# Performance work log

Hardware: AMD Instinct MI355X
Metric: run time of the kernel (lower is better)

## Reference

```python
import jax, jax.numpy as jnp
import numpy as np

N_SIGMA = 1
K_INST = 8  # instance ids 1..K_INST (0 = background)
W_INST, W_VAR, W_SEED = 1.0, 10.0, 1.0
FG_WEIGHT = 1.0


def make_xym(h, w):
    # torch buffer: linspace(0,2,2048) x / linspace(0,1,1024) y, sliced to [0:h,0:w]
    xm = jnp.linspace(0.0, 2.0, 2048)[:w]
    ym = jnp.linspace(0.0, 1.0, 1024)[:h]
    return jnp.stack([jnp.broadcast_to(xm[None, :], (h, w)),
                      jnp.broadcast_to(ym[:, None], (h, w))], axis=0)  # [2,h,w]


def lovasz_hinge_flat(logits, labels):
    # logits, labels: [N] float (labels in {0,1})
    signs = 2.0 * labels - 1.0
    errors = 1.0 - logits * signs
    order = jnp.argsort(-errors)            # descending sort of errors
    errors_sorted = errors[order]
    gt_sorted = labels[order]
    gts = gt_sorted.sum()
    inter = gts - jnp.cumsum(gt_sorted)
    union = gts + jnp.cumsum(1.0 - gt_sorted)
    jac = 1.0 - inter / union
    grad = jnp.concatenate([jac[:1], jac[1:] - jac[:-1]])
    # torch impl wraps grad in Variable() -> no gradient through grad
    return jnp.dot(jax.nn.relu(errors_sorted), jax.lax.stop_gradient(grad))


def spatial_emb_loss(predictions, instances):
    B, C, T, h, w = predictions.shape
    xym = make_xym(h, w)
    # Faithful to the torch source: due to loop indentation, only the last
    # time step's var/instance/seed losses survive, and obj_count == 1.
    pred = predictions[:, :, T - 1]          # [B,C,h,w]
    inst = instances[:, 0, T - 1]            # [B,h,w] int
    spatial_emb = jnp.tanh(pred[:, 0:2]) + xym[None]   # [B,2,h,w]
    sigma = pred[:, 2:2 + N_SIGMA]                     # [B,1,h,w]
    seed = jax.nn.sigmoid(pred[:, 2 + N_SIGMA])        # [B,h,w]
    npix = float(h * w)

    def per_image(se, sig, sd, ins):
        bg_loss = jnp.sum(jnp.where(ins == 0, sd ** 2, 0.0))

        def per_id(k):
            m = (ins == k).astype(se.dtype)            # [h,w]
            cnt = m.sum()
            safe = jnp.maximum(cnt, 1.0)
            # to_center=True: center of in-mask pixel coordinates
            center = jnp.sum(xym * m[None], axis=(1, 2)) / safe      # [2]
            s_mean = jnp.sum(sig * m[None], axis=(1, 2)) / safe      # [n_sigma]
            var_l = jnp.sum(m[None] * (sig - jax.lax.stop_gradient(s_mean)[:, None, None]) ** 2) / (safe * N_SIGMA)
            s_exp = jnp.exp(s_mean * 10.0)
            dist = jnp.exp(-jnp.sum((se - center[:, None, None]) ** 2 * s_exp[:, None, None], axis=0))  # [h,w]
            inst_l = lovasz_hinge_flat((dist * 2.0 - 1.0).reshape(-1), m.reshape(-1))
            seed_l = FG_WEIGHT * jnp.sum(m * (sd - jax.lax.stop_gradient(dist)) ** 2)
            present = (cnt > 0).astype(se.dtype)       # torch skips absent ids
            return present * var_l, present * inst_l, present * seed_l

        var_l, inst_l, seed_l = jax.vmap(per_id)(jnp.arange(1, K_INST + 1))
        seed_loss = (bg_loss + seed_l.sum()) / npix
        # obj_count == 1 in the original code (incremented once per t-loop)
        return W_INST * inst_l.sum() + W_VAR * var_l.sum() + W_SEED * seed_loss

    per_b = jax.vmap(per_image)(spatial_emb, sigma, seed, inst)
    # torch: loss = loss / b, with b == B-1 after the loop
    return per_b.sum() / (B - 1)


def setup_inputs():
    key = jax.random.key(0)
    k1, k2 = jax.random.split(key)
    B, C, T, H, W = 4, 4, 2, 512, 1024
    predictions = jax.random.normal(k1, (B, C, T, H, W), dtype=jnp.float32)
    instances = jax.random.randint(k2, (B, 1, T, H, W), 0, K_INST + 1, dtype=jnp.int32)
    labels = jnp.zeros((B, 1, T, H, W), dtype=jnp.int32)  # unused by forward
    return {"predictions": predictions, "instances": instances, "labels": labels}


def reference(predictions, instances, labels):
    return spatial_emb_loss(predictions, instances)
```

## Files before the change

kernel.cpp:

```cpp
#include <hip/hip_runtime.h>

#define H 512
#define WID 1024
#define HW (H*WID)
#define B 4
#define K 8
#define NB 1024
#define NBLK1 128

#define OFF_LOSS  0
#define OFF_FIN   16
#define OFF_SPART 512
#define OFF_RED   (OFF_SPART + B*K*NBLK1*5)
#define OFF_PART  (OFF_RED + 2*B*K*NB)

static __device__ __forceinline__ float frcp(float x){
#if __has_builtin(__builtin_amdgcn_rcpf)
  return __builtin_amdgcn_rcpf(x);
#else
  return 1.0f / x;
#endif
}
static __device__ __forceinline__ float fexp2(float x){
#if __has_builtin(__builtin_amdgcn_exp2f)
  return __builtin_amdgcn_exp2f(x);
#else
  return exp2f(x);
#endif
}
static __device__ __forceinline__ float ftanh(float x){
  return 1.0f - 2.0f * frcp(__expf(2.0f*x) + 1.0f);
}
static __device__ __forceinline__ float fsigmoid(float x){
  return frcp(1.0f + __expf(-x));
}

__global__ __launch_bounds__(512) void k1_stats(const float* __restrict__ pred,
                                                const int* __restrict__ inst,
                                                float* __restrict__ ws) {
  const int b = blockIdx.y;
  __shared__ int4   ti[1024];
  __shared__ float4 ts[1024];
  __shared__ float  part5[K][5];
  const float4* sig4 = (const float4*)(pred + (size_t)(8*b + 5) * HW);
  const int4*   ins4 = (const int4*)(inst + (size_t)(2*b + 1) * HW);
  const int base4 = blockIdx.x * 1024;
  #pragma unroll
  for (int i = 0; i < 2; i++) {
    const int q = threadIdx.x + i*512;
    ti[q] = ins4[base4 + q];
    ts[q] = sig4[base4 + q];
  }
  __syncthreads();
  const int wv = threadIdx.x >> 6, lane = threadIdx.x & 63;
  const int kk = wv + 1;
  float cnt=0.f, sx=0.f, sy=0.f, ss=0.f, ss2=0.f;
  #pragma unroll
  for (int j = 0; j < 16; j++) {
    const int q = lane + 64*j;
    const int4   iv = ti[q];
    const float4 sv = ts[q];
    const int p = (base4 + q) * 4;
    const float xm0 = (float)(p & (WID-1)) * (2.0f/2047.0f);
    const float ym  = (float)(p >> 10)     * (1.0f/1023.0f);
    const float m0 = (iv.x==kk)?1.f:0.f, m1=(iv.y==kk)?1.f:0.f,
                m2 = (iv.z==kk)?1.f:0.f, m3=(iv.w==kk)?1.f:0.f;
    const float msum = (m0+m1)+(m2+m3);
    cnt += msum;
    sx  += msum*xm0 + (m1 + 2.0f*m2 + 3.0f*m3)*(2.0f/2047.0f);
    sy  += msum*ym;
    ss  += m0*sv.x + m1*sv.y + m2*sv.z + m3*sv.w;
    ss2 += m0*sv.x*sv.x + m1*sv.y*sv.y + m2*sv.z*sv.z + m3*sv.w*sv.w;
  }
  #pragma unroll
  for (int o=1;o<64;o<<=1){
    cnt+=__shfl_xor(cnt,o,64);
    sx +=__shfl_xor(sx, o,64);
    sy +=__shfl_xor(sy, o,64);
    ss +=__shfl_xor(ss, o,64);
    ss2+=__shfl_xor(ss2,o,64);
  }
  if (lane == 0) {
    part5[wv][0]=cnt; part5[wv][1]=sx; part5[wv][2]=sy; part5[wv][3]=ss; part5[wv][4]=ss2;
  }
  __syncthreads();
  if (threadIdx.x < K*5) {
    const int w = threadIdx.x / 5, c = threadIdx.x % 5;
    ws[OFF_SPART + ((size_t)(b*K + w)*NBLK1 + blockIdx.x)*5 + c] = part5[w][c];
  }
}

__global__ __launch_bounds__(256) void k2_fin(float* __restrict__ ws) {
  const int t = threadIdx.x;
  const int bk = t >> 3, s = t & 7;
  float a0=0.f,a1=0.f,a2=0.f,a3=0.f,a4=0.f;
  for (int j = 0; j < NBLK1/8; j++) {
    const float* p = ws + OFF_SPART + ((size_t)bk*NBLK1 + (s + 8*j))*5;
    a0+=p[0]; a1+=p[1]; a2+=p[2]; a3+=p[3]; a4+=p[4];
  }
  #pragma unroll
  for (int o=1;o<8;o<<=1){
    a0+=__shfl_xor(a0,o,64); a1+=__shfl_xor(a1,o,64); a2+=__shfl_xor(a2,o,64);
    a3+=__shfl_xor(a3,o,64); a4+=__shfl_xor(a4,o,64);
  }
  __shared__ float vloc[32];
  if (s == 0) {
    const float cnt=a0, sx=a1, sy=a2, ss=a3, ss2=a4;
    const float present = (cnt > 0.0f) ? 1.0f : 0.0f;
    const float safe = fmaxf(cnt, 1.0f);
    const float cx = sx/safe, cy = sy/safe, sm = ss/safe;
    const float var = (ss2 - 2.0f*sm*ss + sm*sm*cnt)/safe;
    const float sexp = expf(10.0f * sm);
    const float L2E = 1.4426950408889634f;
    float* fin = ws + OFF_FIN + bk*8;
    fin[0] = -sexp*L2E;
    fin[1] =  2.0f*sexp*cx*L2E;
    fin[2] =  2.0f*sexp*cy*L2E;
    fin[3] = -sexp*(cx*cx + cy*cy)*L2E + 10.0f;
    fin[4] = cnt;
    vloc[bk] = present * 10.0f * var * (1.0f/3.0f);
  }
  __syncthreads();
  if (t == 0) {
    float v = 0.f;
    #pragma unroll
    for (int i = 0; i < 32; i++) v += vloc[i];
    atomicAdd(ws + OFF_LOSS, v);
  }
}

template<int G>
__global__ __launch_bounds__(256, 4) void k3_main(const float* __restrict__ pred,
                                                  const int* __restrict__ inst,
                                                  float* __restrict__ ws,
                                                  unsigned int* __restrict__ part) {
  const int b = blockIdx.y, g = blockIdx.x;
  __shared__ unsigned int hist[K*NB];
  for (int i = threadIdx.x; i < K*NB; i += 256) hist[i] = 0;
  float4 fr[K];
  #pragma unroll
  for (int k=0;k<K;k++){
    const float* fin = ws + OFF_FIN + (b*K + k)*8;
    fr[k] = make_float4(fin[0], fin[1], fin[2], fin[3]);
  }
  __syncthreads();
  const float4* p0 = (const float4*)(pred + (size_t)(8*b+1)*HW);
  const float4* p1 = (const float4*)(pred + (size_t)(8*b+3)*HW);
  const float4* p3 = (const float4*)(pred + (size_t)(8*b+7)*HW);
  const int4*   in4 = (const int4*)(inst + (size_t)(2*b+1)*HW);
  float sAcc = 0.0f;
  constexpr int CH4 = HW / (G*4);
  const int base4 = g * CH4;
  #pragma unroll
  for (int q0 = 0; q0 < CH4; q0 += 256) {
    const int idx = base4 + q0 + threadIdx.x;
    const int4   iv = in4[idx];
    const float4 f0 = p0[idx];
    const float4 f1 = p1[idx];
    const float4 f3 = p3[idx];
    const int p = idx * 4;
    const float xm0 = (float)(p & (WID-1)) * (2.0f/2047.0f);
    const float ym  = (float)(p >> 10)     * (1.0f/1023.0f);
    const int ivv[4] = {iv.x, iv.y, iv.z, iv.w};
    float pxv[4], pyv[4], t2v[4], down[4];
    {
      const float a0v[4] = {f0.x, f0.y, f0.z, f0.w};
      const float a1v[4] = {f1.x, f1.y, f1.z, f1.w};
      #pragma unroll
      for (int e=0;e<4;e++){
        pxv[e] = ftanh(a0v[e]) + xm0 + (float)e*(2.0f/2047.0f);
        pyv[e] = ftanh(a1v[e]) + ym;
        t2v[e] = pxv[e]*pxv[e] + pyv[e]*pyv[e];
        down[e] = 0.0f;
      }
    }
    #pragma unroll
    for (int j=0;j<K;j++){
      const float4 f = fr[j];
      int buv[4]; unsigned addv[4];
      #pragma unroll
      for (int e=0;e<4;e++){
        const float u = fmaf(f.x, t2v[e], fmaf(f.y, pxv[e], fmaf(f.z, pyv[e], f.w)));
        const float v = fexp2(u);
        int vi = (int)v; vi = (vi > NB-1) ? NB-1 : vi;
        const bool own = (ivv[e] == j+1);
        if (own) down[e] = v;
        buv[e] = own ? (NB-1 - vi) : vi;
        addv[e] = own ? 0x10001u : 1u;
      }
      int cur = buv[0]; unsigned acc = addv[0];
      #pragma unroll
      for (int e=1;e<4;e++){
        const bool same = (buv[e] == cur);
        if (!same) atomicAdd(&hist[j*NB + cur], acc);
        acc = same ? acc + addv[e] : addv[e];
        cur = buv[e];
      }
      atomicAdd(&hist[j*NB + cur], acc);
    }
    {
      const float sdv[4] = {fsigmoid(f3.x), fsigmoid(f3.y), fsigmoid(f3.z), fsigmoid(f3.w)};
      #pragma unroll
      for (int e=0;e<4;e++){
        const float d  = (ivv[e] == 0) ? 0.0f : down[e] * (1.0f/1024.0f);
        const float df = sdv[e] - d;
        sAcc += df*df;
      }
    }
  }
  __syncthreads();
  unsigned int* dst = part + ((size_t)b*G + g)*(K*NB);
  for (int i = threadIdx.x; i < K*NB; i += 256) dst[i] = hist[i];
  #pragma unroll
  for (int o=1;o<64;o<<=1) sAcc += __shfl_xor(sAcc, o, 64);
  __shared__ float wsum[4];
  if ((threadIdx.x & 63) == 0) wsum[threadIdx.x>>6] = sAcc;
  __syncthreads();
  if (threadIdx.x == 0) {
    const float tot = wsum[0]+wsum[1]+wsum[2]+wsum[3];
    atomicAdd(ws + OFF_LOSS, tot * (1.0f/((float)HW * 3.0f)));
  }
}

__global__ __launch_bounds__(128) void k4a_reduce(const unsigned int* __restrict__ part,
                                                  unsigned int* __restrict__ red, int G) {
  const int bk = blockIdx.x, c = blockIdx.y;
  const int b = bk >> 3, k = bk & 7;
  const int bu = c*128 + threadIdx.x;
  const unsigned int* base = part + (size_t)b*G*K*NB + (size_t)k*NB + bu;
  unsigned int rc = 0, rp = 0;
  #pragma unroll 8
  for (int g = 0; g < G; g++) {
    const unsigned int v = base[(size_t)g*K*NB];
    rc += v & 0xFFFFu;
    rp += v >> 16;
  }
  red[bk*NB + bu]            = rc;
  red[B*K*NB + bk*NB + bu]   = rp;
}

__global__ __launch_bounds__(256) void k4b_lovasz(const unsigned int* __restrict__ red,
                                                   float* __restrict__ ws) {
  const int bk = blockIdx.x;
  const float cntF = ws[OFF_FIN + bk*8 + 4];
  if (cntF <= 0.0f) return;
  const double Pd = (double)cntF;
  const int t = threadIdx.x;
  const int lane = t & 63, wv = t >> 6;
  unsigned int cnt[4], pos[4];
  #pragma unroll
  for (int j = 0; j < 4; j++) {
    const int bu = NB-1 - (t*4 + j);
    cnt[j] = red[bk*NB + bu];
    pos[j] = red[B*K*NB + bk*NB + bu];
  }
  const int lc = (int)(cnt[0]+cnt[1]+cnt[2]+cnt[3]);
  const int lp = (int)(pos[0]+pos[1]+pos[2]+pos[3]);
  int ic = lc, ip = lp;
  #pragma unroll
  for (int o=1;o<64;o<<=1){
    const int vc = __shfl_up(ic, o, 64);
    const int vp = __shfl_up(ip, o, 64);
    if (lane >= o) { ic += vc; ip += vp; }
  }
  __shared__ int wtc[4], wtp[4];
  if (lane == 63) { wtc[wv] = ic; wtp[wv] = ip; }
  __syncthreads();
  int offc = 0, offp = 0;
  for (int w = 0; w < wv; w++) { offc += wtc[w]; offp += wtp[w]; }
  int irun = offc + ic - lc;
  int crun = offp + ip - lp;
  double acc = 0.0;
  #pragma unroll
  for (int j = 0; j < 4; j++) {
    const int n = (int)cnt[j];
    if (n) {
      const int bu = NB-1 - (t*4 + j);
      const double jac0 = (irun==0) ? 0.0 : 1.0 - (Pd - crun)/(Pd + irun - crun);
      irun += n; crun += (int)pos[j];
      const double jac1 = 1.0 - (Pd - crun)/(Pd + irun - crun);
      acc += ((bu + 0.5) * (2.0/NB)) * (jac1 - jac0);
    }
  }
  #pragma unroll
  for (int o=1;o<64;o<<=1) acc += __shfl_xor(acc, o, 64);
  __shared__ double racc[4];
  if (lane == 0) racc[wv] = acc;
  __syncthreads();
  if (t == 0) {
    const double tot = racc[0]+racc[1]+racc[2]+racc[3];
    atomicAdd(ws + OFF_LOSS, (float)(tot * (1.0/3.0)));
  }
}

__global__ void k5_out(const float* __restrict__ ws, float* __restrict__ out) {
  if (threadIdx.x == 0) out[0] = ws[OFF_LOSS];
}

extern "C" void kernel_launch(void* const* d_in, const int* in_sizes, int n_in,
                              void* d_out, int out_size, void* d_ws, size_t ws_size,
                              hipStream_t stream) {
  const float* pred = (const float*)d_in[0];
  const int*   inst = (const int*)d_in[1];
  float* ws  = (float*)d_ws;
  float* out = (float*)d_out;
  unsigned int* red  = ((unsigned int*)d_ws) + OFF_RED;
  unsigned int* part = ((unsigned int*)d_ws) + OFF_PART;
  int G = 256;
  while (G > 32 && ws_size < ((size_t)OFF_PART + (size_t)B*G*K*NB)*4) G >>= 1;
  hipMemsetAsync(d_ws, 0, (size_t)OFF_FIN*4 + 64, stream);
  k1_stats<<<dim3(NBLK1,B), 512, 0, stream>>>(pred, inst, ws);
  k2_fin  <<<1, 256, 0, stream>>>(ws);
  if      (G == 256) k3_main<256><<<dim3(256,B), 256, 0, stream>>>(pred, inst, ws, part);
  else if (G == 128) k3_main<128><<<dim3(128,B), 256, 0, stream>>>(pred, inst, ws, part);
  else if (G ==  64) k3_main< 64><<<dim3( 64,B), 256, 0, stream>>>(pred, inst, ws, part);
  else               k3_main< 32><<<dim3( 32,B), 256, 0, stream>>>(pred, inst, ws, part);
  k4a_reduce<<<dim3(B*K, 8), 128, 0, stream>>>(part, red, G);
  k4b_lovasz<<<B*K, 256, 0, stream>>>(red, ws);
  k5_out  <<<1, 64, 0, stream>>>(ws, out);
}
```

Before: 149.1 us.

## Fold stats finalize into main kernel, fuse output write, use 512-thread blocks

Removes the separate k2_fin launch: each k3_main block now reduces the k1 partial stats itself (one wave per instance id) and derives its coefficients in shared memory. The final output copy moves into k4b_lovasz through a last-block ticket counter, which drops the k5 launch. The main kernel goes from 256 to 512 threads with half as many blocks, and histogram init and copy use vector stores. The cost is that every k3 block repeats the finalize work, and the larger blocks change occupancy.

```diff
diff --git a/kernel.cpp b/kernel.cpp
--- a/kernel.cpp
+++ b/kernel.cpp
@@ -9,9 +9,10 @@
 #define NBLK1 128
 
 #define OFF_LOSS  0
+#define OFF_TICK  1
 #define OFF_FIN   16
 #define OFF_SPART 512
-#define OFF_RED   (OFF_SPART + B*K*NBLK1*5)
+#define OFF_RED   (OFF_SPART + B*K*NBLK1*8)
 #define OFF_PART  (OFF_RED + 2*B*K*NB)
 
 static __device__ __forceinline__ float frcp(float x){
@@ -84,66 +85,57 @@
     part5[wv][0]=cnt; part5[wv][1]=sx; part5[wv][2]=sy; part5[wv][3]=ss; part5[wv][4]=ss2;
   }
   __syncthreads();
-  if (threadIdx.x < K*5) {
-    const int w = threadIdx.x / 5, c = threadIdx.x % 5;
-    ws[OFF_SPART + ((size_t)(b*K + w)*NBLK1 + blockIdx.x)*5 + c] = part5[w][c];
-  }
-}
-
-__global__ __launch_bounds__(256) void k2_fin(float* __restrict__ ws) {
-  const int t = threadIdx.x;
-  const int bk = t >> 3, s = t & 7;
-  float a0=0.f,a1=0.f,a2=0.f,a3=0.f,a4=0.f;
-  for (int j = 0; j < NBLK1/8; j++) {
-    const float* p = ws + OFF_SPART + ((size_t)bk*NBLK1 + (s + 8*j))*5;
-    a0+=p[0]; a1+=p[1]; a2+=p[2]; a3+=p[3]; a4+=p[4];
-  }
-  #pragma unroll
-  for (int o=1;o<8;o<<=1){
-    a0+=__shfl_xor(a0,o,64); a1+=__shfl_xor(a1,o,64); a2+=__shfl_xor(a2,o,64);
-    a3+=__shfl_xor(a3,o,64); a4+=__shfl_xor(a4,o,64);
-  }
-  __shared__ float vloc[32];
-  if (s == 0) {
-    const float cnt=a0, sx=a1, sy=a2, ss=a3, ss2=a4;
-    const float present = (cnt > 0.0f) ? 1.0f : 0.0f;
-    const float safe = fmaxf(cnt, 1.0f);
-    const float cx = sx/safe, cy = sy/safe, sm = ss/safe;
-    const float var = (ss2 - 2.0f*sm*ss + sm*sm*cnt)/safe;
-    const float sexp = expf(10.0f * sm);
-    const float L2E = 1.4426950408889634f;
-    float* fin = ws + OFF_FIN + bk*8;
-    fin[0] = -sexp*L2E;
-    fin[1] =  2.0f*sexp*cx*L2E;
-    fin[2] =  2.0f*sexp*cy*L2E;
-    fin[3] = -sexp*(cx*cx + cy*cy)*L2E + 10.0f;
-    fin[4] = cnt;
-    vloc[bk] = present * 10.0f * var * (1.0f/3.0f);
-  }
-  __syncthreads();
-  if (t == 0) {
-    float v = 0.f;
-    #pragma unroll
-    for (int i = 0; i < 32; i++) v += vloc[i];
-    atomicAdd(ws + OFF_LOSS, v);
+  if (threadIdx.x < K*8) {
+    const int w = threadIdx.x >> 3, c = threadIdx.x & 7;
+    if (c < 5)
+      ws[OFF_SPART + ((size_t)(b*K + w)*NBLK1 + blockIdx.x)*8 + c] = part5[w][c];
   }
 }
 
 template<int G>
-__global__ __launch_bounds__(256, 4) void k3_main(const float* __restrict__ pred,
+__global__ __launch_bounds__(512, 4) void k3_main(const float* __restrict__ pred,
                                                   const int* __restrict__ inst,
                                                   float* __restrict__ ws,
                                                   unsigned int* __restrict__ part) {
   const int b = blockIdx.y, g = blockIdx.x;
   __shared__ unsigned int hist[K*NB];
-  for (int i = threadIdx.x; i < K*NB; i += 256) hist[i] = 0;
+  __shared__ float4 finL[K];
+  __shared__ float  vlocL[K];
+  for (int i = threadIdx.x*4; i < K*NB; i += 512*4)
+    *(uint4*)&hist[i] = make_uint4(0u,0u,0u,0u);
+  const int wv = threadIdx.x >> 6, lane = threadIdx.x & 63;
+  {
+    const float* p = ws + OFF_SPART + (size_t)(b*K + wv)*NBLK1*8;
+    const float4 q0 = *(const float4*)(p + (size_t)lane*8);
+    const float  e0 = p[(size_t)lane*8 + 4];
+    const float4 q1 = *(const float4*)(p + (size_t)(lane+64)*8);
+    const float  e1 = p[(size_t)(lane+64)*8 + 4];
+    float a0=q0.x+q1.x, a1=q0.y+q1.y, a2=q0.z+q1.z, a3=q0.w+q1.w, a4=e0+e1;
+    #pragma unroll
+    for (int o=1;o<64;o<<=1){
+      a0+=__shfl_xor(a0,o,64); a1+=__shfl_xor(a1,o,64); a2+=__shfl_xor(a2,o,64);
+      a3+=__shfl_xor(a3,o,64); a4+=__shfl_xor(a4,o,64);
+    }
+    if (lane == 0) {
+      const float cnt=a0, sx=a1, sy=a2, ss=a3, ss2=a4;
+      const float present = (cnt > 0.0f) ? 1.0f : 0.0f;
+      const float safe = fmaxf(cnt, 1.0f);
+      const float cx = sx/safe, cy = sy/safe, sm = ss/safe;
+      const float var = (ss2 - 2.0f*sm*ss + sm*sm*cnt)/safe;
+      const float sexp = expf(10.0f * sm);
+      const float L2E = 1.4426950408889634f;
+      finL[wv] = make_float4(-sexp*L2E,
+                              2.0f*sexp*cx*L2E,
+                              2.0f*sexp*cy*L2E,
+                             -sexp*(cx*cx + cy*cy)*L2E + 10.0f);
+      vlocL[wv] = present * 10.0f * var * (1.0f/3.0f);
+      if (g == 0) ws[OFF_FIN + (b*K + wv)*8 + 4] = cnt;
+    }
+  }
+  __syncthreads();
   float4 fr[K];
   #pragma unroll
-  for (int k=0;k<K;k++){
-    const float* fin = ws + OFF_FIN + (b*K + k)*8;
-    fr[k] = make_float4(fin[0], fin[1], fin[2], fin[3]);
-  }
-  __syncthreads();
+  for (int k=0;k<K;k++) fr[k] = finL[k];
   const float4* p0 = (const float4*)(pred + (size_t)(8*b+1)*HW);
   const float4* p1 = (const float4*)(pred + (size_t)(8*b+3)*HW);
   const float4* p3 = (const float4*)(pred + (size_t)(8*b+7)*HW);
@@ -152,7 +144,7 @@
   constexpr int CH4 = HW / (G*4);
   const int base4 = g * CH4;
   #pragma unroll
-  for (int q0 = 0; q0 < CH4; q0 += 256) {
+  for (int q0 = 0; q0 < CH4; q0 += 512) {
     const int idx = base4 + q0 + threadIdx.x;
     const int4   iv = in4[idx];
     const float4 f0 = p0[idx];
@@ -210,15 +202,23 @@
   }
   __syncthreads();
   unsigned int* dst = part + ((size_t)b*G + g)*(K*NB);
-  for (int i = threadIdx.x; i < K*NB; i += 256) dst[i] = hist[i];
+  for (int i = threadIdx.x*4; i < K*NB; i += 512*4)
+    *(uint4*)&dst[i] = *(const uint4*)&hist[i];
   #pragma unroll
   for (int o=1;o<64;o<<=1) sAcc += __shfl_xor(sAcc, o, 64);
-  __shared__ float wsum[4];
-  if ((threadIdx.x & 63) == 0) wsum[threadIdx.x>>6] = sAcc;
+  __shared__ float wsum[8];
+  if (lane == 0) wsum[wv] = sAcc;
   __syncthreads();
   if (threadIdx.x == 0) {
-    const float tot = wsum[0]+wsum[1]+wsum[2]+wsum[3];
-    atomicAdd(ws + OFF_LOSS, tot * (1.0f/((float)HW * 3.0f)));
+    float tot = 0.f;
+    #pragma unroll
+    for (int w = 0; w < 8; w++) tot += wsum[w];
+    float add = tot * (1.0f/((float)HW * 3.0f));
+    if (g == 0) {
+      #pragma unroll
+      for (int k = 0; k < K; k++) add += vlocL[k];
+    }
+    atomicAdd(ws + OFF_LOSS, add);
   }
 }
 
@@ -240,61 +240,68 @@
 }
 
 __global__ __launch_bounds__(256) void k4b_lovasz(const unsigned int* __restrict__ red,
-                                                   float* __restrict__ ws) {
+                                                   float* __restrict__ ws,
+                                                   float* __restrict__ out) {
   const int bk = blockIdx.x;
   const float cntF = ws[OFF_FIN + bk*8 + 4];
-  if (cntF <= 0.0f) return;
-  const double Pd = (double)cntF;
   const int t = threadIdx.x;
-  const int lane = t & 63, wv = t >> 6;
-  unsigned int cnt[4], pos[4];
-  #pragma unroll
-  for (int j = 0; j < 4; j++) {
-    const int bu = NB-1 - (t*4 + j);
-    cnt[j] = red[bk*NB + bu];
-    pos[j] = red[B*K*NB + bk*NB + bu];
-  }
-  const int lc = (int)(cnt[0]+cnt[1]+cnt[2]+cnt[3]);
-  const int lp = (int)(pos[0]+pos[1]+pos[2]+pos[3]);
-  int ic = lc, ip = lp;
-  #pragma unroll
-  for (int o=1;o<64;o<<=1){
-    const int vc = __shfl_up(ic, o, 64);
-    const int vp = __shfl_up(ip, o, 64);
-    if (lane >= o) { ic += vc; ip += vp; }
-  }
-  __shared__ int wtc[4], wtp[4];
-  if (lane == 63) { wtc[wv] = ic; wtp[wv] = ip; }
-  __syncthreads();
-  int offc = 0, offp = 0;
-  for (int w = 0; w < wv; w++) { offc += wtc[w]; offp += wtp[w]; }
-  int irun = offc + ic - lc;
-  int crun = offp + ip - lp;
-  double acc = 0.0;
-  #pragma unroll
-  for (int j = 0; j < 4; j++) {
-    const int n = (int)cnt[j];
-    if (n) {
+  if (cntF > 0.0f) {
+    const double Pd = (double)cntF;
+    const int lane = t & 63, wv = t >> 6;
+    unsigned int cnt[4], pos[4];
+    #pragma unroll
+    for (int j = 0; j < 4; j++) {
       const int bu = NB-1 - (t*4 + j);
-      const double jac0 = (irun==0) ? 0.0 : 1.0 - (Pd - crun)/(Pd + irun - crun);
-      irun += n; crun += (int)pos[j];
-      const double jac1 = 1.0 - (Pd - crun)/(Pd + irun - crun);
-      acc += ((bu + 0.5) * (2.0/NB)) * (jac1 - jac0);
-    }
-  }
-  #pragma unroll
-  for (int o=1;o<64;o<<=1) acc += __shfl_xor(acc, o, 64);
-  __shared__ double racc[4];
-  if (lane == 0) racc[wv] = acc;
-  __syncthreads();
+      cnt[j] = red[bk*NB + bu];
+      pos[j] = red[B*K*NB + bk*NB + bu];
+    }
+    const int lc = (int)(cnt[0]+cnt[1]+cnt[2]+cnt[3]);
+    const int lp = (int)(pos[0]+pos[1]+pos[2]+pos[3]);
+    int ic = lc, ip = lp;
+    #pragma unroll
+    for (int o=1;o<64;o<<=1){
+      const int vc = __shfl_up(ic, o, 64);
+      const int vp = __shfl_up(ip, o, 64);
+      if (lane >= o) { ic += vc; ip += vp; }
+    }
+    __shared__ int wtc[4], wtp[4];
+    if (lane == 63) { wtc[wv] = ic; wtp[wv] = ip; }
+    __syncthreads();
+    int offc = 0, offp = 0;
+    for (int w = 0; w < wv; w++) { offc += wtc[w]; offp += wtp[w]; }
+    int irun = offc + ic - lc;
+    int crun = offp + ip - lp;
+    double acc = 0.0;
+    #pragma unroll
+    for (int j = 0; j < 4; j++) {
+      const int n = (int)cnt[j];
+      if (n) {
+        const int bu = NB-1 - (t*4 + j);
+        const double jac0 = (irun==0) ? 0.0 : 1.0 - (Pd - crun)/(Pd + irun - crun);
+        irun += n; crun += (int)pos[j];
+        const double jac1 = 1.0 - (Pd - crun)/(Pd + irun - crun);
+        acc += ((bu + 0.5) * (2.0/NB)) * (jac1 - jac0);
+      }
+    }
+    #pragma unroll
+    for (int o=1;o<64;o<<=1) acc += __shfl_xor(acc, o, 64);
+    __shared__ double racc[4];
+    if (lane == 0) racc[wv] = acc;
+    __syncthreads();
+    if (t == 0) {
+      const double tot = racc[0]+racc[1]+racc[2]+racc[3];
+      atomicAdd(ws + OFF_LOSS, (float)(tot * (1.0/3.0)));
+    }
+  }
   if (t == 0) {
-    const double tot = racc[0]+racc[1]+racc[2]+racc[3];
-    atomicAdd(ws + OFF_LOSS, (float)(tot * (1.0/3.0)));
-  }
-}
-
-__global__ void k5_out(const float* __restrict__ ws, float* __restrict__ out) {
-  if (threadIdx.x == 0) out[0] = ws[OFF_LOSS];
+    __threadfence();
+    unsigned int* wsu = (unsigned int*)ws;
+    const unsigned int old = atomicAdd(&wsu[OFF_TICK], 1u);
+    if (old == (unsigned)(B*K - 1)) {
+      __threadfence();
+      out[0] = *((volatile float*)(ws + OFF_LOSS));
+    }
+  }
 }
 
 extern "C" void kernel_launch(void* const* d_in, const int* in_sizes, int n_in,
@@ -306,16 +313,13 @@
   float* out = (float*)d_out;
   unsigned int* red  = ((unsigned int*)d_ws) + OFF_RED;
   unsigned int* part = ((unsigned int*)d_ws) + OFF_PART;
-  int G = 256;
+  int G = 128;
   while (G > 32 && ws_size < ((size_t)OFF_PART + (size_t)B*G*K*NB)*4) G >>= 1;
-  hipMemsetAsync(d_ws, 0, (size_t)OFF_FIN*4 + 64, stream);
+  hipMemsetAsync(d_ws, 0, 128, stream);
   k1_stats<<<dim3(NBLK1,B), 512, 0, stream>>>(pred, inst, ws);
-  k2_fin  <<<1, 256, 0, stream>>>(ws);
-  if      (G == 256) k3_main<256><<<dim3(256,B), 256, 0, stream>>>(pred, inst, ws, part);
-  else if (G == 128) k3_main<128><<<dim3(128,B), 256, 0, stream>>>(pred, inst, ws, part);
-  else if (G ==  64) k3_main< 64><<<dim3( 64,B), 256, 0, stream>>>(pred, inst, ws, part);
-  else               k3_main< 32><<<dim3( 32,B), 256, 0, stream>>>(pred, inst, ws, part);
+  if      (G == 128) k3_main<128><<<dim3(128,B), 512, 0, stream>>>(pred, inst, ws, part);
+  else if (G ==  64) k3_main< 64><<<dim3( 64,B), 512, 0, stream>>>(pred, inst, ws, part);
+  else               k3_main< 32><<<dim3( 32,B), 512, 0, stream>>>(pred, inst, ws, part);
   k4a_reduce<<<dim3(B*K, 8), 128, 0, stream>>>(part, red, G);
-  k4b_lovasz<<<B*K, 256, 0, stream>>>(red, ws);
-  k5_out  <<<1, 64, 0, stream>>>(ws, out);
-}
+  k4b_lovasz<<<B*K, 256, 0, stream>>>(red, ws, out);
+}
```

Result: faster. 137.6 us (-7.7%).
